# Kernel tuning notes

Hardware: AMD Instinct MI355X
Metric: run time of the kernel (lower is better)

## Reference

```python
import jax, jax.numpy as jnp
import numpy as np

# ---- module hyperparameters ----
B, L, F = 128, 720, 128
SEG = 24            # segment_length
NSEG = L // SEG     # 30 input segments
WIN = 15            # window_size
NPRED = 96 // SEG   # 4 prediction segments
D = 128             # encode_dim
H = 512             # hidden_dim
DECAY = 0.9
C = 1.0             # curvature
EPS = 1e-6
MAXN = 1.0 - 1e-5   # max radius of Poincare ball (c=1)
SQC = 1.0           # sqrt(C)

# ---- Poincare-ball manifold ops ----
def _sqnorm(x):
    return jnp.sum(x * x, axis=-1, keepdims=True)

def _norm(x):
    return jnp.sqrt(jnp.maximum(_sqnorm(x), EPS * EPS))

def _project(x):
    n = _norm(x)
    return jnp.where(n > MAXN, x * (MAXN / n), x)

def _artanh(x):
    return jnp.arctanh(jnp.clip(x, -1.0 + 1e-7, 1.0 - 1e-7))

def mobius_add(x, y):
    xy = jnp.sum(x * y, axis=-1, keepdims=True)
    x2, y2 = _sqnorm(x), _sqnorm(y)
    num = (1.0 + 2.0 * C * xy + C * y2) * x + (1.0 - C * x2) * y
    den = 1.0 + 2.0 * C * xy + C * C * x2 * y2
    return num / jnp.maximum(den, EPS)

def expmap0(v):
    n = _norm(v)
    return _project(jnp.tanh(SQC * n) * v / (SQC * n))

def logmap0(y):
    n = _norm(y)
    return _artanh(SQC * n) * y / (SQC * n)

def expmap(x, v):
    lam = 2.0 / jnp.maximum(1.0 - C * _sqnorm(x), EPS)
    n = _norm(v)
    second = jnp.tanh(SQC * lam * n / 2.0) * v / (SQC * n)
    return _project(mobius_add(x, second))

def logmap(x, y):
    d = mobius_add(-x, y)
    n = _norm(d)
    lam = 2.0 / jnp.maximum(1.0 - C * _sqnorm(x), EPS)
    return (2.0 / (SQC * lam)) * _artanh(SQC * n) * d / n


def setup_inputs() -> dict:
    key = jax.random.key(0)
    ks = jax.random.split(key, 12)
    s = 0.05
    return {
        'trend':           0.5 * jax.random.normal(ks[0], (B, L, F), jnp.float32),
        'seasonal_coarse': 0.5 * jax.random.normal(ks[1], (B, L, F), jnp.float32),
        'seasonal_fine':   0.5 * jax.random.normal(ks[2], (B, L, F), jnp.float32),
        'residual':        0.5 * jax.random.normal(ks[3], (B, L, F), jnp.float32),
        'W_t': s * jax.random.normal(ks[4], (SEG, D), jnp.float32), 'b_t': jnp.zeros((D,), jnp.float32),
        'W_c': s * jax.random.normal(ks[5], (SEG, D), jnp.float32), 'b_c': jnp.zeros((D,), jnp.float32),
        'W_f': s * jax.random.normal(ks[6], (SEG, D), jnp.float32), 'b_f': jnp.zeros((D,), jnp.float32),
        'W_r': s * jax.random.normal(ks[7], (SEG, D), jnp.float32), 'b_r': jnp.zeros((D,), jnp.float32),
        'alpha': jnp.array([0.5], jnp.float32),
        'W1': s * jax.random.normal(ks[8], (D, H), jnp.float32), 'b1': jnp.zeros((H,), jnp.float32),
        'W2': s * jax.random.normal(ks[9], (H, SEG), jnp.float32), 'b2': jnp.zeros((SEG,), jnp.float32),
    }


def reference(trend, seasonal_coarse, seasonal_fine, residual,
              W_t, b_t, W_c, b_c, W_f, b_f, W_r, b_r,
              alpha, W1, b1, W2, b2):
    b, l, f = trend.shape

    def collapse(x):  # [B,L,F] -> [B*F, NSEG, SEG]
        return x.transpose(0, 2, 1).reshape(b * f, NSEG, SEG)

    t_s, c_s, f_s, r_s = map(collapse, (trend, seasonal_coarse, seasonal_fine, residual))

    # per-segment tangent encoding (channel-independent, shared params)
    tan = (jnp.einsum('bns,sd->bnd', t_s, W_t) + b_t
           + jnp.einsum('bns,sd->bnd', c_s, W_c) + b_c
           + jnp.einsum('bns,sd->bnd', f_s, W_f) + b_f
           + jnp.einsum('bns,sd->bnd', r_s, W_r) + b_r)
    z = expmap0(tan)                     # [BF, NSEG, D] on the ball
    z_cur = z[:, -WIN:, :]

    idx = jnp.arange(WIN - 1, dtype=jnp.float32)
    w = DECAY ** (WIN - 2 - idx)
    w = w / w.sum()

    preds, latents = [], []
    for _ in range(NPRED):
        z_last = z_cur[:, -1]
        vel = logmap(z_cur[:, :-1], z_cur[:, 1:])
        avg_v = jnp.sum(vel * w[None, :, None], axis=1)    # [BF, D]
        z_next = expmap(z_last, alpha * avg_v)             # dynamics step
        latents.append(z_next)
        # reconstruction head: logmap0 -> MLP -> segment
        t0 = logmap0(z_next)
        seg = jax.nn.relu(t0 @ W1 + b1) @ W2 + b2          # [BF, SEG]
        preds.append(seg)
        z_cur = jnp.concatenate([z_cur[:, 1:], z_next[:, None]], axis=1)

    p = jnp.stack(preds, axis=1).reshape(b * f, NPRED * SEG)
    predictions = p.reshape(b, f, NPRED * SEG).transpose(0, 2, 1)  # [B, pred_len, F]
    return predictions
```

## Files before the change

### kernel.cpp

```cpp
#include <hip/hip_runtime.h>
#include <hip/hip_bf16.h>

namespace {
constexpr int kL = 720, kF = 128;
constexpr int kWin = 15;
constexpr float kEps = 1e-6f;
constexpr float kMaxN = 1.0f - 1e-5f;
constexpr int kT0off = 360;
constexpr int ZTR = 132;
constexpr int AROW = 104;
constexpr size_t kOffT0   = 0;
constexpr size_t kOffW1   = 16777216;
constexpr size_t kOffW2   = kOffW1 + 131072;
constexpr size_t kOffBt   = kOffW2 + 32768;
constexpr size_t kOffBsum = kOffBt + 73728;
}

typedef float f32x4 __attribute__((ext_vector_type(4)));
typedef short s16x8 __attribute__((ext_vector_type(8)));

__device__ __forceinline__ float rcp_f(float x) { return __builtin_amdgcn_rcpf(x); }
__device__ __forceinline__ float sqrt_f(float x) { return __builtin_amdgcn_sqrtf(x); }
__device__ __forceinline__ float tanh_f(float x) {
  float t = __builtin_amdgcn_exp2f(x * -2.8853900817779268f);
  return (1.0f - t) * rcp_f(1.0f + t);
}
__device__ __forceinline__ float artanh_f(float n) {
  float nc = fminf(n, 1.0f - 1e-7f);
  return 0.34657359027997264f * __builtin_amdgcn_logf((1.0f + nc) * rcp_f(1.0f - nc));
}

template<int CTRL>
__device__ __forceinline__ float dpp_add(float v) {
  int mv = __builtin_amdgcn_update_dpp(0, __float_as_int(v), CTRL, 0xF, 0xF, false);
  return v + __int_as_float(mv);
}
__device__ __forceinline__ float sum16(float v) {
  v = dpp_add<0xB1>(v);
  v = dpp_add<0x4E>(v);
  v = dpp_add<0x141>(v);
  v = dpp_add<0x128>(v);
  return v;
}
__device__ __forceinline__ float sum64(float v) {
  v = sum16(v);
  v += __shfl_xor(v, 16);
  v += __shfl_xor(v, 32);
  return v;
}
__device__ __forceinline__ float rlane(float v, int i) {
  return __int_as_float(__builtin_amdgcn_readlane(__float_as_int(v), i));
}

extern "C" __global__ __launch_bounds__(256)
void mwhf_prep(const float* __restrict__ W1, const float* __restrict__ W2,
               const float* __restrict__ W_t, const float* __restrict__ W_c,
               const float* __restrict__ W_f, const float* __restrict__ W_r,
               const float* __restrict__ b_t, const float* __restrict__ b_c,
               const float* __restrict__ b_f, const float* __restrict__ b_r,
               __hip_bfloat16* __restrict__ W1bf, __hip_bfloat16* __restrict__ W2bf,
               __hip_bfloat16* __restrict__ BtH, __hip_bfloat16* __restrict__ BtM,
               __hip_bfloat16* __restrict__ BtL, float* __restrict__ bsum)
{
  const int b = blockIdx.x, tid = threadIdx.x;
  if (b < 64) {
    const int n0 = b * 8;
    for (int e = tid; e < 1024; e += 256) {
      int n_l = e & 7, k = e >> 3;
      W1bf[(size_t)(n0 + n_l) * 128 + k] = __float2bfloat16(W1[(size_t)k * 512 + n0 + n_l]);
    }
  } else if (b < 68) {
    const int k0 = (b - 64) * 128;
    for (int e = tid; e < 4096; e += 256) {
      int p = e >> 7, k_l = e & 127;
      float v = (p < 24) ? W2[(size_t)(k0 + k_l) * 24 + p] : 0.0f;
      W2bf[(size_t)p * 512 + k0 + k_l] = __float2bfloat16(v);
    }
  } else if (b < 72) {
    const int st = b - 68;
    const float* src = (st == 0) ? W_t : (st == 1) ? W_c : (st == 2) ? W_f : W_r;
    for (int e = tid; e < 3072; e += 256) {
      int s = e >> 7, d = e & 127;
      float x = src[e];
      __hip_bfloat16 h = __float2bfloat16(x);
      float r1 = x - __bfloat162float(h);
      __hip_bfloat16 m = __float2bfloat16(r1);
      float r2 = r1 - __bfloat162float(m);
      const int o = d * 96 + st * 24 + s;
      BtH[o] = h;
      BtM[o] = m;
      BtL[o] = __float2bfloat16(r2);
    }
  } else {
    if (tid < 128) bsum[tid] = b_t[tid] + b_c[tid] + b_f[tid] + b_r[tid];
  }
}

extern "C" __global__ __launch_bounds__(256, 4)
void mwhf_k1(const float* __restrict__ trend,
             const float* __restrict__ seas_c,
             const float* __restrict__ seas_f,
             const float* __restrict__ resid,
             const __hip_bfloat16* __restrict__ BtH,
             const __hip_bfloat16* __restrict__ BtM,
             const __hip_bfloat16* __restrict__ BtL,
             const float* __restrict__ bsum,
             const float* __restrict__ alpha,
             __hip_bfloat16* __restrict__ t0_out)
{
  __shared__ __align__(16) char smem_raw[3 * 64 * AROW * 2];
  __shared__ float z2s[80];
  __shared__ float pds[80];

  float* ublk = (float*)smem_raw;
  __hip_bfloat16* Ah = (__hip_bfloat16*)smem_raw;
  __hip_bfloat16* Am = Ah + 64 * AROW;
  __hip_bfloat16* Al = Am + 64 * AROW;

  const int tid = threadIdx.x;
  const int bix = blockIdx.x;
  const int bb = (bix & 7) * 16 + (bix >> 8);
  const int f0 = ((bix >> 3) & 31) * 4;
  const int row0 = bb * 128 + f0;

  for (int e = tid; e < 192; e += 256) {
    int rr = e / 48, cc = e - rr * 48;
    int off = (rr * 16 + 15) * AROW;
    ((unsigned int*)(Ah + off))[cc] = 0u;
    ((unsigned int*)(Am + off))[cc] = 0u;
    ((unsigned int*)(Al + off))[cc] = 0u;
  }
  {
    const float* ptrs[4] = {trend, seas_c, seas_f, resid};
    for (int e = tid; e < 1440; e += 256) {
      int seg = e / 96;
      int k = e - seg * 96;
      int st = k / 24, s = k - st * 24;
      const float* p = ptrs[st];
      float4 v = *(const float4*)&p[(size_t)(bb * kL + kT0off + seg * 24 + s) * kF + f0];
      float xv[4] = {v.x, v.y, v.z, v.w};
#pragma unroll
      for (int f = 0; f < 4; ++f) {
        int m = f * 16 + seg;
        __hip_bfloat16 h = __float2bfloat16(xv[f]);
        float r1 = xv[f] - __bfloat162float(h);
        __hip_bfloat16 mm = __float2bfloat16(r1);
        float r2 = r1 - __bfloat162float(mm);
        Ah[m * AROW + k] = h;
        Am[m * AROW + k] = mm;
        Al[m * AROW + k] = __float2bfloat16(r2);
      }
    }
  }
  __syncthreads();

  const int w = tid >> 6;
  const int lane = tid & 63;
  const int l16 = lane & 15, quad = lane >> 4;

  f32x4 acc0[8];
  float scale4[4], zz4[4];
  {
    s16x8 ah[3], am[3], al[3];
    const int abase = (w * 16 + l16) * AROW + quad * 8;
#pragma unroll
    for (int ks = 0; ks < 3; ++ks) {
      ah[ks] = *(const s16x8*)(Ah + abase + ks * 32);
      am[ks] = *(const s16x8*)(Am + abase + ks * 32);
      al[ks] = *(const s16x8*)(Al + abase + ks * 32);
    }
#pragma unroll
    for (int t = 0; t < 8; ++t) acc0[t] = (f32x4)0.f;
    const __hip_bfloat16* bhp = BtH + l16 * 96 + quad * 8;
    const __hip_bfloat16* bmp = BtM + l16 * 96 + quad * 8;
    const __hip_bfloat16* blp = BtL + l16 * 96 + quad * 8;
#pragma unroll
    for (int t = 0; t < 8; ++t) {
#pragma unroll
      for (int ks = 0; ks < 3; ++ks) {
        s16x8 bh = *(const s16x8*)(bhp + t * 1536 + ks * 32);
        s16x8 bm = *(const s16x8*)(bmp + t * 1536 + ks * 32);
        s16x8 bl = *(const s16x8*)(blp + t * 1536 + ks * 32);
        acc0[t] = __builtin_amdgcn_mfma_f32_16x16x32_bf16(ah[ks], bh, acc0[t], 0, 0, 0);
        acc0[t] = __builtin_amdgcn_mfma_f32_16x16x32_bf16(am[ks], bh, acc0[t], 0, 0, 0);
        acc0[t] = __builtin_amdgcn_mfma_f32_16x16x32_bf16(ah[ks], bm, acc0[t], 0, 0, 0);
        acc0[t] = __builtin_amdgcn_mfma_f32_16x16x32_bf16(al[ks], bh, acc0[t], 0, 0, 0);
        acc0[t] = __builtin_amdgcn_mfma_f32_16x16x32_bf16(ah[ks], bl, acc0[t], 0, 0, 0);
        acc0[t] = __builtin_amdgcn_mfma_f32_16x16x32_bf16(am[ks], bm, acc0[t], 0, 0, 0);
      }
    }
    float part[4] = {0.f, 0.f, 0.f, 0.f};
#pragma unroll
    for (int t = 0; t < 8; ++t) {
      float bv = bsum[t * 16 + l16];
#pragma unroll
      for (int r = 0; r < 4; ++r) {
        float v = acc0[t][r] + bv;
        acc0[t][r] = v;
        part[r] += v * v;
      }
    }
#pragma unroll
    for (int r = 0; r < 4; ++r) part[r] = sum16(part[r]);
#pragma unroll
    for (int r = 0; r < 4; ++r) {
      float v2 = part[r];
      float nv = sqrt_f(fmaxf(v2, 1e-12f));
      float sc = tanh_f(nv) * rcp_f(nv);
      float y2 = sc * sc * v2;
      float yn = sqrt_f(fmaxf(y2, 1e-12f));
      float proj = (yn > kMaxN) ? (kMaxN * rcp_f(yn)) : 1.0f;
      scale4[r] = sc * proj;
      zz4[r] = y2 * proj * proj;
    }
  }
  __syncthreads();
  {
#pragma unroll
    for (int r = 0; r < 4; ++r) {
      int row = quad * 4 + r;
      if (row < kWin) {
#pragma unroll
        for (int t = 0; t < 8; ++t)
          ublk[(w * kWin + row) * ZTR + t * 16 + l16] = acc0[t][r] * scale4[r];
        if (l16 == 0) z2s[w * 20 + row] = zz4[r];
      }
    }
  }
  __syncthreads();

  {
    const int l = lane;
    float zx[19], zy[19];
#pragma unroll
    for (int j = 0; j < 15; ++j) {
      float2 v = *(const float2*)&ublk[(w * kWin + j) * ZTR + 2 * l];
      zx[j] = v.x; zy[j] = v.y;
    }
    {
      float pd[14];
#pragma unroll
      for (int j = 0; j < 14; ++j) pd[j] = zx[j] * zx[j + 1] + zy[j] * zy[j + 1];
#pragma unroll
      for (int j = 0; j < 14; ++j) pd[j] = sum64(pd[j]);
      if (l == 0) {
#pragma unroll
        for (int j = 0; j < 14; ++j) pds[w * 20 + j] = pd[j];
      }
    }
    const float alp = alpha[0];
    const float cw14 = (l < 14)
        ? __builtin_amdgcn_exp2f((float)(13 - l) * -0.15200309344504997f) * 0.12966260f
        : 0.f;
#pragma unroll
    for (int it = 0; it < 4; ++it) {
      float cA = 0.f, cB = 0.f, cW = 0.f;
      if (l < 14) {
        float dp = pds[w * 20 + it + l];
        float x2 = z2s[w * 20 + it + l];
        float y2 = z2s[w * 20 + it + l + 1];
        cA = 1.f - 2.f * dp + y2;
        cB = 1.f - x2;
        float den = fmaxf(1.f - 2.f * dp + x2 * y2, kEps);
        float invd = rcp_f(den);
        float d2 = (cA * cA * x2 - 2.f * cA * cB * dp + cB * cB * y2) * (invd * invd);
        float n = sqrt_f(fmaxf(d2, 1e-12f));
        float coef = fmaxf(cB, kEps) * artanh_f(n) * rcp_f(n);
        cW = cw14 * coef * invd;
      }
      float avx = 0.f, avy = 0.f;
#pragma unroll
      for (int i = 0; i < 14; ++i) {
        float sA = rlane(cA, i), sB = rlane(cB, i), sW = rlane(cW, i);
        float tx = sB * zx[it + i + 1] - sA * zx[it + i];
        float ty = sB * zy[it + i + 1] - sA * zy[it + i];
        avx += sW * tx;
        avy += sW * ty;
      }
      float vx = alp * avx, vy = alp * avy;
      const int pl = it + 14;
      float x2l = z2s[w * 20 + pl];
      float v2 = vx * vx + vy * vy;
      float xdv = zx[pl] * vx + zy[pl] * vy;
      v2 = sum64(v2);
      xdv = sum64(xdv);
      float nv = sqrt_f(fmaxf(v2, 1e-12f));
      float lam = 2.f * rcp_f(fmaxf(1.f - x2l, kEps));
      float co = tanh_f(0.5f * lam * nv) * rcp_f(nv);
      float s2 = co * co * v2;
      float xy = co * xdv;
      float P = 1.f + 2.f * xy + s2;
      float Q = 1.f - x2l;
      float den2 = fmaxf(1.f + 2.f * xy + x2l * s2, kEps);
      float invd2 = rcp_f(den2);
      float znx = (P * zx[pl] + Q * co * vx) * invd2;
      float zny = (P * zy[pl] + Q * co * vy) * invd2;
      float zn2 = (P * P * x2l + 2.f * P * Q * xy + Q * Q * s2) * (invd2 * invd2);
      float pdn = (P * x2l + Q * xy) * invd2;
      float yn = sqrt_f(fmaxf(zn2, 1e-12f));
      float proj = (yn > kMaxN) ? (kMaxN * rcp_f(yn)) : 1.f;
      znx *= proj; zny *= proj;
      zn2 *= proj * proj;
      pdn *= proj;
      zx[15 + it] = znx; zy[15 + it] = zny;
      if (l == 0) {
        z2s[w * 20 + 15 + it] = zn2;
        pds[w * 20 + 14 + it] = pdn;
      }
      float n0 = sqrt_f(fmaxf(zn2, 1e-12f));
      float fac = artanh_f(n0) * rcp_f(n0);
      __hip_bfloat162 hv;
      hv.x = __float2bfloat16(fac * znx);
      hv.y = __float2bfloat16(fac * zny);
      *(__hip_bfloat162*)(t0_out + ((size_t)(row0 + w) * 4 + it) * 128 + 2 * l) = hv;
    }
  }
}

extern "C" __global__ __launch_bounds__(256, 4)
void mwhf_k2g(const __hip_bfloat16* __restrict__ t0g,
              const __hip_bfloat16* __restrict__ W1bf,
              const __hip_bfloat16* __restrict__ W2bf,
              const float* __restrict__ b1, const float* __restrict__ b2,
              float* __restrict__ outp)
{
  __shared__ __align__(16) __hip_bfloat16 hids[32 * 512];
  s16x8* hidv = (s16x8*)hids;

  const int tid = threadIdx.x;
  const int w = tid >> 6, lane = tid & 63;
  const int l16 = lane & 15, quad = lane >> 4;
  const int mbase = blockIdx.x * 32;
  const int ng = w * 128;

  s16x8 afr[2][4];
#pragma unroll
  for (int s = 0; s < 2; ++s)
#pragma unroll
    for (int kc = 0; kc < 4; ++kc)
      afr[s][kc] = *(const s16x8*)(t0g + (size_t)(mbase + s * 16 + l16) * 128 + kc * 32 + quad * 8);

  f32x4 acc[2][8];
#pragma unroll
  for (int s = 0; s < 2; ++s)
#pragma unroll
    for (int t = 0; t < 8; ++t) acc[s][t] = (f32x4)0.f;

#pragma unroll
  for (int t = 0; t < 8; ++t) {
    const __hip_bfloat16* bp = W1bf + (size_t)(ng + t * 16 + l16) * 128 + quad * 8;
#pragma unroll
    for (int kc = 0; kc < 4; ++kc) {
      s16x8 bfr = *(const s16x8*)(bp + kc * 32);
      acc[0][t] = __builtin_amdgcn_mfma_f32_16x16x32_bf16(afr[0][kc], bfr, acc[0][t], 0, 0, 0);
      acc[1][t] = __builtin_amdgcn_mfma_f32_16x16x32_bf16(afr[1][kc], bfr, acc[1][t], 0, 0, 0);
    }
  }
#pragma unroll
  for (int t = 0; t < 8; ++t) {
    const int nl = ng + t * 16 + l16;
    float bv = b1[nl];
#pragma unroll
    for (int s = 0; s < 2; ++s)
#pragma unroll
      for (int r = 0; r < 4; ++r) {
        int m = s * 16 + quad * 4 + r;
        float h = fmaxf(acc[s][t][r] + bv, 0.f);
        hids[m * 512 + (nl ^ ((m & 7) << 3))] = __float2bfloat16(h);
      }
  }
  __syncthreads();

  {
    const int s2i = w & 1, t2 = w >> 1;
    f32x4 a2 = (f32x4)0.f;
    const int mrow = s2i * 16 + l16;
#pragma unroll 4
    for (int kc = 0; kc < 16; ++kc) {
      s16x8 av = hidv[mrow * 64 + ((kc * 4 + quad) ^ (l16 & 7))];
      s16x8 bfr = *(const s16x8*)(W2bf + (size_t)(t2 * 16 + l16) * 512 + kc * 32 + quad * 8);
      a2 = __builtin_amdgcn_mfma_f32_16x16x32_bf16(av, bfr, a2, 0, 0, 0);
    }
    const int p = t2 * 16 + l16;
    if (p < 24) {
      float bv = b2[p];
#pragma unroll
      for (int r = 0; r < 4; ++r) {
        int m = mbase + s2i * 16 + quad * 4 + r;
        int bbi = m >> 9, it = m & 3, f = (m >> 2) & 127;
        outp[(size_t)bbi * 12288 + (it * 24 + p) * 128 + f] = a2[r] + bv;
      }
    }
  }
}

extern "C" void kernel_launch(void* const* d_in, const int* in_sizes, int n_in,
                              void* d_out, int out_size, void* d_ws, size_t ws_size,
                              hipStream_t stream) {
  (void)in_sizes; (void)n_in; (void)out_size; (void)ws_size;
  const float* trend = (const float*)d_in[0];
  const float* sc    = (const float*)d_in[1];
  const float* sf    = (const float*)d_in[2];
  const float* rs    = (const float*)d_in[3];
  const float* W_t   = (const float*)d_in[4];
  const float* b_t   = (const float*)d_in[5];
  const float* W_c   = (const float*)d_in[6];
  const float* b_c   = (const float*)d_in[7];
  const float* W_f   = (const float*)d_in[8];
  const float* b_f   = (const float*)d_in[9];
  const float* W_r   = (const float*)d_in[10];
  const float* b_r   = (const float*)d_in[11];
  const float* alpha = (const float*)d_in[12];
  const float* W1    = (const float*)d_in[13];
  const float* b1    = (const float*)d_in[14];
  const float* W2    = (const float*)d_in[15];
  const float* b2    = (const float*)d_in[16];

  char* ws = (char*)d_ws;
  __hip_bfloat16* t0   = (__hip_bfloat16*)(ws + kOffT0);
  __hip_bfloat16* W1bf = (__hip_bfloat16*)(ws + kOffW1);
  __hip_bfloat16* W2bf = (__hip_bfloat16*)(ws + kOffW2);
  __hip_bfloat16* BtH  = (__hip_bfloat16*)(ws + kOffBt);
  __hip_bfloat16* BtM  = BtH + 12288;
  __hip_bfloat16* BtL  = BtM + 12288;
  float* bsum = (float*)(ws + kOffBsum);
  float* outp = (float*)d_out;

  hipLaunchKernelGGL(mwhf_prep, dim3(73), dim3(256), 0, stream,
                     W1, W2, W_t, W_c, W_f, W_r, b_t, b_c, b_f, b_r,
                     W1bf, W2bf, BtH, BtM, BtL, bsum);
  hipLaunchKernelGGL(mwhf_k1, dim3(4096), dim3(256), 0, stream,
                     trend, sc, sf, rs, BtH, BtM, BtL, bsum, alpha, t0);
  hipLaunchKernelGGL(mwhf_k2g, dim3(2048), dim3(256), 0, stream,
                     t0, W1bf, W2bf, b1, b2, outp);
}
```

Baseline: 365.3 us.

## Split encoder and dynamics into separate kernels with global latent buffer

Replaces the fused encode+dynamics kernel with two kernels when the workspace is large enough. The first tiles by (segment, batch), stages 96 input rows for all features in LDS and runs a split-bf16 MFMA projection with expmap0. It writes latents and their squared norms to a ~126MB workspace buffer. The second reads those per row and runs the four hyperbolic dynamics steps with wave reductions. This aims at better load coalescing and MFMA reuse across features, at the cost of a large global round trip for the latent tensor.

After: 374.8 us. 2.6% more time.

```diff
diff --git a/kernel.cpp b/kernel.cpp
--- a/kernel.cpp
+++ b/kernel.cpp
@@ -9,11 +9,15 @@
 constexpr int kT0off = 360;
 constexpr int ZTR = 132;
 constexpr int AROW = 104;
+constexpr int XR = 129;
 constexpr size_t kOffT0   = 0;
 constexpr size_t kOffW1   = 16777216;
 constexpr size_t kOffW2   = kOffW1 + 131072;
 constexpr size_t kOffBt   = kOffW2 + 32768;
 constexpr size_t kOffBsum = kOffBt + 73728;
+constexpr size_t kOffZ2   = 17018880;
+constexpr size_t kOffZ    = 18874368;
+constexpr size_t kWsNew   = kOffZ + 125829120;
 }
 
 typedef float f32x4 __attribute__((ext_vector_type(4)));
@@ -50,6 +54,12 @@
 }
 __device__ __forceinline__ float rlane(float v, int i) {
   return __int_as_float(__builtin_amdgcn_readlane(__float_as_int(v), i));
+}
+__device__ __forceinline__ unsigned short rne_bf16(float f, float& fval) {
+  unsigned u = __float_as_uint(f);
+  unsigned r = (u + 0x7FFFu + ((u >> 16) & 1u)) & 0xFFFF0000u;
+  fval = __uint_as_float(r);
+  return (unsigned short)(r >> 16);
 }
 
 extern "C" __global__ __launch_bounds__(256)
@@ -93,6 +103,229 @@
     }
   } else {
     if (tid < 128) bsum[tid] = b_t[tid] + b_c[tid] + b_f[tid] + b_r[tid];
+  }
+}
+
+extern "C" __global__ __launch_bounds__(256, 3)
+void mwhf_k1a2(const float* __restrict__ trend,
+               const float* __restrict__ seas_c,
+               const float* __restrict__ seas_f,
+               const float* __restrict__ resid,
+               const __hip_bfloat16* __restrict__ BtH,
+               const __hip_bfloat16* __restrict__ BtM,
+               const __hip_bfloat16* __restrict__ BtL,
+               const float* __restrict__ bsum,
+               float* __restrict__ z_ws, float* __restrict__ z2_ws)
+{
+  __shared__ __align__(16) float X[96 * XR];
+
+  const int tid = threadIdx.x;
+  const int seg = blockIdx.x;
+  const int bb  = blockIdx.y;
+
+  {
+    const float* ptrs[4] = {trend, seas_c, seas_f, resid};
+#pragma unroll
+    for (int it = 0; it < 12; ++it) {
+      int e = it * 256 + tid;
+      int row = e >> 5;
+      int fq = (e & 31) * 4;
+      int st = row / 24, sI = row - st * 24;
+      float4 v = *(const float4*)&ptrs[st][(size_t)(bb * kL + kT0off + seg * 24 + sI) * kF + fq];
+      float* dst = &X[row * XR + fq];
+      dst[0] = v.x; dst[1] = v.y; dst[2] = v.z; dst[3] = v.w;
+    }
+  }
+  __syncthreads();
+
+  const int w = tid >> 6, lane = tid & 63;
+  const int l16 = lane & 15, quad = lane >> 4;
+  const int fbase = w * 32;
+
+  f32x4 acc[2][8];
+#pragma unroll
+  for (int s = 0; s < 2; ++s)
+#pragma unroll
+    for (int t = 0; t < 8; ++t) acc[s][t] = (f32x4)0.f;
+
+  const __hip_bfloat16* bhp = BtH + l16 * 96 + quad * 8;
+  const __hip_bfloat16* bmp = BtM + l16 * 96 + quad * 8;
+  const __hip_bfloat16* blp = BtL + l16 * 96 + quad * 8;
+
+#pragma unroll
+  for (int ks = 0; ks < 3; ++ks) {
+    s16x8 ah[2], am[2], al[2];
+#pragma unroll
+    for (int s = 0; s < 2; ++s) {
+      const int f = fbase + s * 16 + l16;
+      const float* ar = &X[(ks * 32 + quad * 8) * XR + f];
+#pragma unroll
+      for (int j = 0; j < 8; ++j) {
+        float x = ar[j * XR];
+        unsigned hu = __float_as_uint(x) & 0xFFFF0000u;
+        float r1 = x - __uint_as_float(hu);
+        float mf; unsigned short mb = rne_bf16(r1, mf);
+        float r2 = r1 - mf;
+        float lf; unsigned short lb = rne_bf16(r2, lf);
+        (void)lf;
+        ah[s][j] = (short)(hu >> 16);
+        am[s][j] = (short)mb;
+        al[s][j] = (short)lb;
+      }
+    }
+#pragma unroll
+    for (int t = 0; t < 8; ++t) {
+      s16x8 bh = *(const s16x8*)(bhp + t * 1536 + ks * 32);
+      s16x8 bm = *(const s16x8*)(bmp + t * 1536 + ks * 32);
+      s16x8 bl = *(const s16x8*)(blp + t * 1536 + ks * 32);
+#pragma unroll
+      for (int s = 0; s < 2; ++s) {
+        acc[s][t] = __builtin_amdgcn_mfma_f32_16x16x32_bf16(ah[s], bh, acc[s][t], 0, 0, 0);
+        acc[s][t] = __builtin_amdgcn_mfma_f32_16x16x32_bf16(am[s], bh, acc[s][t], 0, 0, 0);
+        acc[s][t] = __builtin_amdgcn_mfma_f32_16x16x32_bf16(ah[s], bm, acc[s][t], 0, 0, 0);
+        acc[s][t] = __builtin_amdgcn_mfma_f32_16x16x32_bf16(al[s], bh, acc[s][t], 0, 0, 0);
+        acc[s][t] = __builtin_amdgcn_mfma_f32_16x16x32_bf16(ah[s], bl, acc[s][t], 0, 0, 0);
+        acc[s][t] = __builtin_amdgcn_mfma_f32_16x16x32_bf16(am[s], bm, acc[s][t], 0, 0, 0);
+      }
+    }
+  }
+
+  float part[2][4] = {{0.f,0.f,0.f,0.f},{0.f,0.f,0.f,0.f}};
+#pragma unroll
+  for (int t = 0; t < 8; ++t) {
+    float bv = bsum[t * 16 + l16];
+#pragma unroll
+    for (int s = 0; s < 2; ++s)
+#pragma unroll
+      for (int r = 0; r < 4; ++r) {
+        float v = acc[s][t][r] + bv;
+        acc[s][t][r] = v;
+        part[s][r] += v * v;
+      }
+  }
+#pragma unroll
+  for (int s = 0; s < 2; ++s)
+#pragma unroll
+    for (int r = 0; r < 4; ++r) part[s][r] = sum16(part[s][r]);
+
+#pragma unroll
+  for (int s = 0; s < 2; ++s)
+#pragma unroll
+    for (int r = 0; r < 4; ++r) {
+      const int f = fbase + s * 16 + quad * 4 + r;
+      float v2 = part[s][r];
+      float nv = sqrt_f(fmaxf(v2, 1e-12f));
+      float sc = tanh_f(nv) * rcp_f(nv);
+      float y2 = sc * sc * v2;
+      float yn = sqrt_f(fmaxf(y2, 1e-12f));
+      float proj = (yn > kMaxN) ? (kMaxN * rcp_f(yn)) : 1.0f;
+      float scl = sc * proj;
+      float* zr = z_ws + (size_t)(bb * 128 + f) * 1920 + seg * 128;
+#pragma unroll
+      for (int t = 0; t < 8; ++t)
+        zr[t * 16 + l16] = acc[s][t][r] * scl;
+      if (l16 == 0) z2_ws[(bb * 128 + f) * 16 + seg] = y2 * proj * proj;
+    }
+}
+
+extern "C" __global__ __launch_bounds__(256, 6)
+void mwhf_k1b(const float* __restrict__ z_ws, const float* __restrict__ z2_ws,
+              const float* __restrict__ alpha,
+              __hip_bfloat16* __restrict__ t0_out)
+{
+  __shared__ float z2s[80];
+  __shared__ float pds[80];
+  const int tid = threadIdx.x;
+  const int w = tid >> 6, l = tid & 63;
+  const int ro = blockIdx.x * 4 + w;
+
+  float zx[19], zy[19];
+  const float* zr = z_ws + (size_t)ro * 1920;
+#pragma unroll
+  for (int j = 0; j < 15; ++j) {
+    float2 v = *(const float2*)&zr[j * 128 + 2 * l];
+    zx[j] = v.x; zy[j] = v.y;
+  }
+  if (l < 15) z2s[w * 20 + l] = z2_ws[ro * 16 + l];
+
+  {
+    float pd[14];
+#pragma unroll
+    for (int j = 0; j < 14; ++j) pd[j] = zx[j] * zx[j + 1] + zy[j] * zy[j + 1];
+#pragma unroll
+    for (int j = 0; j < 14; ++j) pd[j] = sum64(pd[j]);
+    if (l == 0) {
+#pragma unroll
+      for (int j = 0; j < 14; ++j) pds[w * 20 + j] = pd[j];
+    }
+  }
+
+  const float alp = alpha[0];
+  const float cw14 = (l < 14)
+      ? __builtin_amdgcn_exp2f((float)(13 - l) * -0.15200309344504997f) * 0.12966260f
+      : 0.f;
+
+#pragma unroll
+  for (int it = 0; it < 4; ++it) {
+    float cA = 0.f, cB = 0.f, cW = 0.f;
+    if (l < 14) {
+      float dp = pds[w * 20 + it + l];
+      float x2 = z2s[w * 20 + it + l];
+      float y2 = z2s[w * 20 + it + l + 1];
+      cA = 1.f - 2.f * dp + y2;
+      cB = 1.f - x2;
+      float den = fmaxf(1.f - 2.f * dp + x2 * y2, kEps);
+      float invd = rcp_f(den);
+      float d2 = (cA * cA * x2 - 2.f * cA * cB * dp + cB * cB * y2) * (invd * invd);
+      float n = sqrt_f(fmaxf(d2, 1e-12f));
+      float coef = fmaxf(cB, kEps) * artanh_f(n) * rcp_f(n);
+      cW = cw14 * coef * invd;
+    }
+    float avx = 0.f, avy = 0.f;
+#pragma unroll
+    for (int i = 0; i < 14; ++i) {
+      float sA = rlane(cA, i), sB = rlane(cB, i), sW = rlane(cW, i);
+      float tx = sB * zx[it + i + 1] - sA * zx[it + i];
+      float ty = sB * zy[it + i + 1] - sA * zy[it + i];
+      avx += sW * tx;
+      avy += sW * ty;
+    }
+    float vx = alp * avx, vy = alp * avy;
+    const int pl = it + 14;
+    float x2l = z2s[w * 20 + pl];
+    float v2 = vx * vx + vy * vy;
+    float xdv = zx[pl] * vx + zy[pl] * vy;
+    v2 = sum64(v2);
+    xdv = sum64(xdv);
+    float nv = sqrt_f(fmaxf(v2, 1e-12f));
+    float lam = 2.f * rcp_f(fmaxf(1.f - x2l, kEps));
+    float co = tanh_f(0.5f * lam * nv) * rcp_f(nv);
+    float s2 = co * co * v2;
+    float xy = co * xdv;
+    float P = 1.f + 2.f * xy + s2;
+    float Q = 1.f - x2l;
+    float den2 = fmaxf(1.f + 2.f * xy + x2l * s2, kEps);
+    float invd2 = rcp_f(den2);
+    float znx = (P * zx[pl] + Q * co * vx) * invd2;
+    float zny = (P * zy[pl] + Q * co * vy) * invd2;
+    float zn2 = (P * P * x2l + 2.f * P * Q * xy + Q * Q * s2) * (invd2 * invd2);
+    float pdn = (P * x2l + Q * xy) * invd2;
+    float yn = sqrt_f(fmaxf(zn2, 1e-12f));
+    float proj = (yn > kMaxN) ? (kMaxN * rcp_f(yn)) : 1.f;
+    znx *= proj; zny *= proj;
+    zn2 *= proj * proj;
+    pdn *= proj;
+    zx[15 + it] = znx; zy[15 + it] = zny;
+    if (l == 0) {
+      z2s[w * 20 + 15 + it] = zn2;
+      pds[w * 20 + 14 + it] = pdn;
+    }
+    float n0 = sqrt_f(fmaxf(zn2, 1e-12f));
+    float fac = artanh_f(n0) * rcp_f(n0);
+    __hip_bfloat162 hv;
+    hv.x = __float2bfloat16(fac * znx);
+    hv.y = __float2bfloat16(fac * zny);
+    *(__hip_bfloat162*)(t0_out + ((size_t)ro * 4 + it) * 128 + 2 * l) = hv;
   }
 }
 
@@ -397,7 +630,7 @@
 extern "C" void kernel_launch(void* const* d_in, const int* in_sizes, int n_in,
                               void* d_out, int out_size, void* d_ws, size_t ws_size,
                               hipStream_t stream) {
-  (void)in_sizes; (void)n_in; (void)out_size; (void)ws_size;
+  (void)in_sizes; (void)n_in; (void)out_size;
   const float* trend = (const float*)d_in[0];
   const float* sc    = (const float*)d_in[1];
   const float* sf    = (const float*)d_in[2];
@@ -424,13 +657,22 @@
   __hip_bfloat16* BtM  = BtH + 12288;
   __hip_bfloat16* BtL  = BtM + 12288;
   float* bsum = (float*)(ws + kOffBsum);
+  float* z2w  = (float*)(ws + kOffZ2);
+  float* zw   = (float*)(ws + kOffZ);
   float* outp = (float*)d_out;
 
   hipLaunchKernelGGL(mwhf_prep, dim3(73), dim3(256), 0, stream,
                      W1, W2, W_t, W_c, W_f, W_r, b_t, b_c, b_f, b_r,
                      W1bf, W2bf, BtH, BtM, BtL, bsum);
-  hipLaunchKernelGGL(mwhf_k1, dim3(4096), dim3(256), 0, stream,
-                     trend, sc, sf, rs, BtH, BtM, BtL, bsum, alpha, t0);
+  if (ws_size >= kWsNew) {
+    hipLaunchKernelGGL(mwhf_k1a2, dim3(15, 128), dim3(256), 0, stream,
+                       trend, sc, sf, rs, BtH, BtM, BtL, bsum, zw, z2w);
+    hipLaunchKernelGGL(mwhf_k1b, dim3(4096), dim3(256), 0, stream,
+                       zw, z2w, alpha, t0);
+  } else {
+    hipLaunchKernelGGL(mwhf_k1, dim3(4096), dim3(256), 0, stream,
+                       trend, sc, sf, rs, BtH, BtM, BtL, bsum, alpha, t0);
+  }
   hipLaunchKernelGGL(mwhf_k2g, dim3(2048), dim3(256), 0, stream,
                      t0, W1bf, W2bf, b1, b2, outp);
 }
```
